# Kernel tuning notes

Hardware: AMD Instinct MI355X
Metric: run time of the kernel (lower is better)

## Reference

```python
import jax, jax.numpy as jnp
import numpy as np
import math

B, T, E = 1, 2048, 1024
H = 8                      # num_heads
D = E // H // 2            # head_dim = 64
LAMBDA_INIT = 0.8 - 0.6 * math.exp(-0.3 * 1)  # depth=1
SCALE_BASE = 512.0
THETA = 10000.0


def _rope_tables(T, d):
    # lucidrains rotary-embedding-torch, use_xpos=True, interleaved pairs
    inv_freq = 1.0 / (THETA ** (jnp.arange(0, d, 2, dtype=jnp.float32) / d))
    pos = jnp.arange(T, dtype=jnp.float32)
    freqs = pos[:, None] * inv_freq[None, :]            # (T, d/2)
    freqs = jnp.repeat(freqs, 2, axis=-1)               # (T, d) interleaved
    sv = (jnp.arange(0, d, 2, dtype=jnp.float32) + 0.4 * d) / (1.4 * d)
    power = (pos - T // 2) / SCALE_BASE
    scale = sv[None, :] ** power[:, None]               # (T, d/2)
    scale = jnp.concatenate([scale, scale], axis=-1)    # (T, d)
    return freqs, scale


def _rotate_half(x):
    # interleaved rotate: (..., d) pairs (x1, x2) -> (-x2, x1)
    x1 = x[..., 0::2]
    x2 = x[..., 1::2]
    return jnp.stack([-x2, x1], axis=-1).reshape(x.shape)


def _apply_rope(t, freqs, scale):
    # t: (B, T, h, d); freqs/scale: (T, d) broadcast over heads
    f = freqs[None, :, None, :]
    s = scale[None, :, None, :]
    return t * jnp.cos(f) * s + _rotate_half(t) * jnp.sin(f) * s


def setup_inputs() -> dict:
    key = jax.random.key(0)
    ks = jax.random.split(key, 9)
    w = 0.02
    return {
        "x": jax.random.normal(ks[0], (B, T, E), dtype=jnp.float32),
        "Wq": jax.random.normal(ks[1], (E, E), dtype=jnp.float32) * w,
        "Wk": jax.random.normal(ks[2], (E, E), dtype=jnp.float32) * w,
        "Wv": jax.random.normal(ks[3], (E, E), dtype=jnp.float32) * w,
        "Wo": jax.random.normal(ks[4], (E, E), dtype=jnp.float32) * w,
        "lambda_q1": jax.random.normal(ks[5], (D,), dtype=jnp.float32) * 0.1,
        "lambda_k1": jax.random.normal(ks[6], (D,), dtype=jnp.float32) * 0.1,
        "lambda_q2": jax.random.normal(ks[7], (D,), dtype=jnp.float32) * 0.1,
        "lambda_k2": jax.random.normal(ks[8], (D,), dtype=jnp.float32) * 0.1,
    }


def reference(x, Wq, Wk, Wv, Wo, lambda_q1, lambda_k1, lambda_q2, lambda_k2):
    b, t, e = x.shape
    scaling = D ** -0.5

    q = (x @ Wq.T).reshape(b, t, 2 * H, D)
    k = (x @ Wk.T).reshape(b, t, 2 * H, D)   # n_rep = 1
    v = (x @ Wv.T).reshape(b, t, H, 2 * D)

    freqs, scale = _rope_tables(t, D)
    q = _apply_rope(q, freqs, scale)
    k = _apply_rope(k, freqs, 1.0 / scale)   # xpos: keys use scale**-1

    q = jnp.transpose(q, (0, 2, 1, 3)) * scaling   # (B, 2H, T, D)
    k = jnp.transpose(k, (0, 2, 1, 3))             # (B, 2H, T, D)
    v = jnp.transpose(v, (0, 2, 1, 3))             # (B, H, T, 2D)

    scores = jnp.einsum('bhtd,bhsd->bhts', q, k)
    probs = jax.nn.softmax(scores.astype(jnp.float32), axis=-1).astype(scores.dtype)

    lam1 = jnp.exp(jnp.sum(lambda_q1 * lambda_k1))
    lam2 = jnp.exp(jnp.sum(lambda_q2 * lambda_k2))
    lam = lam1 - lam2 + LAMBDA_INIT

    probs = probs.reshape(b, H, 2, t, t)
    diff = probs[:, :, 0] - lam * probs[:, :, 1]   # (B, H, T, T)

    attn = jnp.einsum('bhts,bhsd->bhtd', diff, v)  # (B, H, T, 2D)
    # RMSNorm (no affine), eps=1e-5
    attn = attn * jax.lax.rsqrt(jnp.mean(attn * attn, axis=-1, keepdims=True) + 1e-5)
    attn = attn * (1.0 - LAMBDA_INIT)

    attn = jnp.transpose(attn, (0, 2, 1, 3)).reshape(b, t, e)
    return attn @ Wo.T
```

## Files before the change

kernel.cpp:

```cpp
#include <hip/hip_runtime.h>
#include <hip/hip_bf16.h>

typedef __hip_bfloat16 bf16;
typedef _Float16 f16;
typedef __attribute__((ext_vector_type(8))) __bf16 bf16x8;
typedef __attribute__((ext_vector_type(8))) _Float16 f16x8;
typedef __attribute__((ext_vector_type(4))) _Float16 f16x4;
typedef __attribute__((ext_vector_type(4))) float floatx4;
typedef __attribute__((ext_vector_type(16))) float floatx16;

#define T_SEQ 2048
#define EMB   1024
#define LAMBDA_INIT 0.35550906759096926f

__device__ __forceinline__ bf16 f2bf(float f) {
  unsigned u;
  __builtin_memcpy(&u, &f, 4);
  u += 0x7FFF + ((u >> 16) & 1);
  unsigned short h = (unsigned short)(u >> 16);
  bf16 r;
  __builtin_memcpy(&r, &h, 2);
  return r;
}

__device__ __forceinline__ int cvtpk_bf16(float lo, float hi) {
  int r;
  asm("v_cvt_pk_bf16_f32 %0, %1, %2" : "=v"(r) : "v"(lo), "v"(hi));
  return r;
}

__device__ __forceinline__ void permswap(int& a, int& b) {
  asm volatile("v_permlane32_swap_b32 %0, %1" : "+v"(a), "+v"(b));
}

__device__ __forceinline__ void gl_lds16(const void* g, void* l) {
  __builtin_amdgcn_global_load_lds((const __attribute__((address_space(1))) void*)g,
                                   (__attribute__((address_space(3))) void*)l, 16, 0, 0);
}

__device__ __forceinline__ floatx4 mfma_h(f16x8 a, f16x8 b, floatx4 c) {
  return __builtin_amdgcn_mfma_f32_16x16x32_f16(a, b, c, 0, 0, 0);
}
__device__ __forceinline__ floatx16 mfma32_h(f16x8 a, f16x8 b, floatx16 c) {
  return __builtin_amdgcn_mfma_f32_32x32x16_f16(a, b, c, 0, 0, 0);
}
__device__ __forceinline__ floatx16 mfma32_bf(bf16x8 a, bf16x8 b, floatx16 c) {
  return __builtin_amdgcn_mfma_f32_32x32x16_bf16(a, b, c, 0, 0, 0);
}

__global__ __launch_bounds__(256) void convert_kernel(
    const float* __restrict__ x,  const float* __restrict__ wq,
    const float* __restrict__ wk, const float* __restrict__ wv,
    const float* __restrict__ wo,
    f16* __restrict__ xf, f16* __restrict__ wqf, f16* __restrict__ wkf,
    f16* __restrict__ wvf, f16* __restrict__ wof)
{
  int b = blockIdx.x;
  const float* src; f16* dst; long off;
  if      (b < 2048) { src = x;  dst = xf;  off = (long)b * 1024; }
  else if (b < 3072) { src = wq; dst = wqf; off = (long)(b - 2048) * 1024; }
  else if (b < 4096) { src = wk; dst = wkf; off = (long)(b - 3072) * 1024; }
  else if (b < 5120) { src = wv; dst = wvf; off = (long)(b - 4096) * 1024; }
  else               { src = wo; dst = wof; off = (long)(b - 5120) * 1024; }
  long i = off + threadIdx.x * 4;
  float4 v = *(const float4*)(src + i);
  f16x4 o;
  o.x = (f16)v.x; o.y = (f16)v.y; o.z = (f16)v.z; o.w = (f16)v.w;
  *(f16x4*)(dst + i) = o;
}

template <int MODE>
__device__ __forceinline__ void gemm64x128_f16(
    const f16* __restrict__ A_, const f16* __restrict__ B_,
    void* C0v, int K, int ldc, int m0, int n0, char* smem)
{
  f16* As = (f16*)smem;
  f16* Bs = (f16*)(smem + 8192);
  const int tid  = threadIdx.x;
  const int wave = tid >> 6, lane = tid & 63, quad = lane >> 4, l16 = lane & 15;
  const int mo = (wave & 1) << 5;
  const int no = (wave >> 1) << 6;

  floatx4 acc[2][4];
  #pragma unroll
  for (int i = 0; i < 2; i++)
    #pragma unroll
    for (int j = 0; j < 4; j++) { acc[i][j][0]=0.f; acc[i][j][1]=0.f; acc[i][j][2]=0.f; acc[i][j][3]=0.f; }

  const int srow = tid >> 3;
  const int ch   = (tid & 7) ^ (srow & 7);
  const long aoff = (long)(m0 + srow) * K + ch * 8;
  const long boff = (long)(n0 + srow) * K + ch * 8;
  const int wb = wave << 10;

  for (int k0 = 0; k0 < K; k0 += 64) {
    #pragma unroll
    for (int rr = 0; rr < 2; rr++)
      gl_lds16(A_ + aoff + k0 + (long)rr * 32 * K, smem + wb + rr * 4096);
    #pragma unroll
    for (int rr = 0; rr < 4; rr++)
      gl_lds16(B_ + boff + k0 + (long)rr * 32 * K, smem + 8192 + wb + rr * 4096);
    __syncthreads();
    #pragma unroll
    for (int kt = 0; kt < 2; kt++) {
      f16x8 a[2], b[4];
      #pragma unroll
      for (int i = 0; i < 2; i++) {
        int m = mo + i * 16 + l16;
        a[i] = *(const f16x8*)(As + m * 64 + ((((kt << 2) | quad) ^ (m & 7)) << 3));
      }
      #pragma unroll
      for (int j = 0; j < 4; j++) {
        int n = no + j * 16 + l16;
        b[j] = *(const f16x8*)(Bs + n * 64 + ((((kt << 2) | quad) ^ (n & 7)) << 3));
      }
      #pragma unroll
      for (int i = 0; i < 2; i++)
        #pragma unroll
        for (int j = 0; j < 4; j++)
          acc[i][j] = mfma_h(a[i], b[j], acc[i][j]);
    }
    __syncthreads();
  }

  if (MODE == 1) {
    #pragma unroll
    for (int i = 0; i < 2; i++)
      #pragma unroll
      for (int j = 0; j < 4; j++)
        #pragma unroll
        for (int r = 0; r < 4; r++) {
          int row = m0 + mo + i * 16 + quad * 4 + r;
          int col = n0 + no + j * 16 + l16;
          ((float*)C0v)[(long)row * ldc + col] = acc[i][j][r];
        }
  } else {
    unsigned short* E = (unsigned short*)smem;
    #pragma unroll
    for (int i = 0; i < 2; i++)
      #pragma unroll
      for (int j = 0; j < 4; j++)
        #pragma unroll
        for (int r = 0; r < 4; r++) {
          int row = mo + i * 16 + quad * 4 + r;
          int col = no + j * 16 + l16;
          float v = acc[i][j][r];
          unsigned short bits;
          if (MODE == 0) {
            bf16 t = f2bf(v);
            __builtin_memcpy(&bits, &t, 2);
          } else {
            float p = __shfl_xor(v, 1, 64);
            int d = col & 63;
            float fr = (float)(m0 + row) * __expf((float)(d >> 1) * -0.28782313662425574f);
            float sn, cs;
            sincosf(fr, &sn, &cs);
            float rot = (col & 1) ? fmaf(v, cs, p * sn) : fmaf(v, cs, -p * sn);
            float power = (float)(m0 + row - 1024) * (1.0f / 512.0f);
            if (MODE == 3) power = -power;
            float sv = fmaf(2.0f, (float)(d & 31), 25.6f) * (1.0f / 89.6f);
            float s = __expf(power * __logf(sv));
            float ov = rot * s;
            if (MODE == 2) ov *= 0.125f;
            f16 t = (f16)ov;
            __builtin_memcpy(&bits, &t, 2);
          }
          E[row * 128 + col] = bits;
        }
    __syncthreads();
    const int rr0 = tid >> 4;
    const int c8  = (tid & 15) * 8;
    #pragma unroll
    for (int p2 = 0; p2 < 4; p2++) {
      int row = p2 * 16 + rr0;
      *(uint4*)((unsigned short*)C0v + (long)(m0 + row) * ldc + n0 + c8) =
          *(const uint4*)(E + row * 128 + c8);
    }
  }
}

__global__ __launch_bounds__(256) void qkv_gemm(
    const f16* __restrict__ xf,
    const f16* __restrict__ wqf, const f16* __restrict__ wkf,
    const f16* __restrict__ wvf,
    f16* __restrict__ qf, f16* __restrict__ kf, bf16* __restrict__ vt)
{
  __shared__ char smem[24576];
  int bid = blockIdx.x;
  if (bid < 256) {
    gemm64x128_f16<2>(xf, wqf, qf, 1024, 1024, (bid >> 3) * 64, (bid & 7) * 128, smem);
  } else if (bid < 512) {
    bid -= 256;
    gemm64x128_f16<3>(xf, wkf, kf, 1024, 1024, (bid >> 3) * 64, (bid & 7) * 128, smem);
  } else {
    bid -= 512;
    gemm64x128_f16<0>(wvf, xf, vt, 1024, 2048, (bid >> 4) * 64, (bid & 15) * 128, smem);
  }
}

__global__ __launch_bounds__(256) void out_gemm(const f16* __restrict__ attn,
                                                const f16* __restrict__ Wo,
                                                float* __restrict__ out)
{
  __shared__ char smem[24576];
  gemm64x128_f16<1>(attn, Wo, out, 1024, 1024,
                    (blockIdx.x >> 3) * 64, (blockIdx.x & 7) * 128, smem);
}

__global__ __launch_bounds__(256) void diff_attn(
    const f16* __restrict__ qf_, const f16* __restrict__ kf_,
    const bf16* __restrict__ vt,
    const float* __restrict__ lq1, const float* __restrict__ lk1,
    const float* __restrict__ lq2, const float* __restrict__ lk2,
    f16* __restrict__ attn)
{
  __shared__ char smem[65536];
  const int tid  = threadIdx.x;
  const int wave = tid >> 6, lane = tid & 63;
  const int l32 = lane & 31, lh = lane >> 5;
  const int h  = blockIdx.x & 7;
  const int qb = blockIdx.x >> 3;
  const int hl = wave >> 1;
  const int ws = wave & 1;
  const int hh = h * 2 + hl;
  const int t0 = qb * 32;

  float a1 = lq1[lane] * lk1[lane];
  float a2 = lq2[lane] * lk2[lane];
  #pragma unroll
  for (int off = 1; off < 64; off <<= 1) {
    a1 += __shfl_xor(a1, off, 64);
    a2 += __shfl_xor(a2, off, 64);
  }
  const float lam = __expf(a1) - __expf(a2) + LAMBDA_INIT;

  f16x8 qfr[4];
  {
    const f16* qrow = qf_ + (long)(t0 + l32) * EMB + hh * 64 + lh * 8;
    #pragma unroll
    for (int kt = 0; kt < 4; kt++) qfr[kt] = *(const f16x8*)(qrow + kt * 16);
  }

  floatx16 o[4];
  #pragma unroll
  for (int nt = 0; nt < 4; nt++)
    #pragma unroll
    for (int r = 0; r < 16; r++) o[nt][r] = 0.f;
  float lr = 0.f;

  const int srow = lane >> 3;
  const int ch   = (lane & 7) ^ srow;
  const f16*  kgp = kf_ + (long)(h * 2 + ws) * 64 + (long)srow * EMB + ch * 8;
  const bf16* vgp = vt + (long)(h * 128 + (wave - 2) * 64 + srow) * T_SEQ + ch * 8;
  const int kofs = wave * 8192;
  const int vofs = 16384 + (wave - 2) * 8192;

  if (wave < 2) {
    #pragma unroll
    for (int j = 0; j < 8; j++)
      gl_lds16(kgp + (long)j * 8 * EMB, smem + kofs + j * 1024);
  } else {
    #pragma unroll
    for (int j = 0; j < 8; j++)
      gl_lds16(vgp + (long)j * 8 * T_SEQ, smem + vofs + j * 1024);
  }

  for (int kb = 0; kb < T_SEQ; kb += 64) {
    const int cur = (kb >> 6) & 1;
    const char* sb = smem + cur * 32768;
    if (kb + 64 < T_SEQ) {
      char* nb = smem + (cur ^ 1) * 32768;
      if (wave < 2) {
        #pragma unroll
        for (int j = 0; j < 8; j++)
          gl_lds16(kgp + (long)(kb + 64) * EMB + (long)j * 8 * EMB,
                   nb + kofs + j * 1024);
      } else {
        #pragma unroll
        for (int j = 0; j < 8; j++)
          gl_lds16(vgp + (kb + 64) + (long)j * 8 * T_SEQ,
                   nb + vofs + j * 1024);
      }
      asm volatile("s_waitcnt vmcnt(8)" ::: "memory");
    } else {
      asm volatile("s_waitcnt vmcnt(0)" ::: "memory");
    }
    asm volatile("s_barrier" ::: "memory");

    const f16*  Ks  = (const f16*)(sb + hl * 8192);
    const bf16* Vsb = (const bf16*)(sb + 16384);

    floatx16 s;
    #pragma unroll
    for (int r = 0; r < 16; r++) s[r] = 0.f;
    #pragma unroll
    for (int kt = 0; kt < 4; kt++) {
      int krow = ws * 32 + l32;
      int c = kt * 2 + lh;
      f16x8 kfr = *(const f16x8*)(Ks + krow * 64 + ((c ^ (krow & 7)) << 3));
      s = mfma32_h(kfr, qfr[kt], s);
    }
    #pragma unroll
    for (int r = 0; r < 16; r++) {
      float pv = __builtin_amdgcn_exp2f(
          fmaf(s[r], 1.4426950408889634f, -17.312340490667562f));
      s[r] = pv;
      lr += pv;
    }
    bf16x8 pf[2];
    #pragma unroll
    for (int kt = 0; kt < 2; kt++) {
      const int b0 = kt * 8;
      int w0 = cvtpk_bf16(s[b0 + 0], s[b0 + 1]);
      int w1 = cvtpk_bf16(s[b0 + 2], s[b0 + 3]);
      int w2 = cvtpk_bf16(s[b0 + 4], s[b0 + 5]);
      int w3 = cvtpk_bf16(s[b0 + 6], s[b0 + 7]);
      permswap(w0, w2);
      permswap(w1, w3);
      union { int i[4]; bf16x8 v; } u;
      u.i[0] = w0; u.i[1] = w1; u.i[2] = w2; u.i[3] = w3;
      pf[kt] = u.v;
    }
    #pragma unroll
    for (int nt = 0; nt < 4; nt++) {
      #pragma unroll
      for (int kt = 0; kt < 2; kt++) {
        int vrow = nt * 32 + l32;
        int c = ws * 4 + kt * 2 + lh;
        bf16x8 vf = *(const bf16x8*)(Vsb + vrow * 64 + ((c ^ (vrow & 7)) << 3));
        o[nt] = mfma32_bf(pf[kt], vf, o[nt]);
      }
    }
    asm volatile("s_barrier" ::: "memory");
  }

  float lrw = lr + __shfl_xor(lr, 32, 64);

  float* Cb = (float*)smem;
  float* Lb = (float*)(smem + 32768);

  if (ws == 1) {
    #pragma unroll
    for (int r = 0; r < 16; r++) {
      int m = (r & 3) + 8 * (r >> 2) + 4 * lh;
      #pragma unroll
      for (int nt = 0; nt < 4; nt++)
        Cb[hl * 4096 + m * 128 + nt * 32 + l32] = o[nt][r];
    }
  }
  if (lh == 0) Lb[ws * 64 + hl * 32 + l32] = lrw;
  __syncthreads();
  if (ws == 0) {
    #pragma unroll
    for (int r = 0; r < 16; r++) {
      int m = (r & 3) + 8 * (r >> 2) + 4 * lh;
      float inv = 1.0f / (Lb[hl * 32 + m] + Lb[64 + hl * 32 + m]);
      #pragma unroll
      for (int nt = 0; nt < 4; nt++)
        o[nt][r] = (o[nt][r] + Cb[hl * 4096 + m * 128 + nt * 32 + l32]) * inv;
    }
  }
  __syncthreads();
  if (hl == 1 && ws == 0) {
    #pragma unroll
    for (int r = 0; r < 16; r++) {
      int m = (r & 3) + 8 * (r >> 2) + 4 * lh;
      #pragma unroll
      for (int nt = 0; nt < 4; nt++)
        Cb[4096 + m * 128 + nt * 32 + l32] = o[nt][r];
    }
  }
  __syncthreads();
  if (hl == 0 && ws == 0) {
    float ss[16];
    #pragma unroll
    for (int r = 0; r < 16; r++) {
      int m = (r & 3) + 8 * (r >> 2) + 4 * lh;
      ss[r] = 0.f;
      #pragma unroll
      for (int nt = 0; nt < 4; nt++) {
        float v = o[nt][r] - lam * Cb[4096 + m * 128 + nt * 32 + l32];
        o[nt][r] = v;
        ss[r] += v * v;
      }
    }
    #pragma unroll
    for (int r = 0; r < 16; r++) {
      ss[r] += __shfl_xor(ss[r], 1, 64);
      ss[r] += __shfl_xor(ss[r], 2, 64);
      ss[r] += __shfl_xor(ss[r], 4, 64);
      ss[r] += __shfl_xor(ss[r], 8, 64);
      ss[r] += __shfl_xor(ss[r], 16, 64);
      float rms = rsqrtf(ss[r] * (1.0f / 128.0f) + 1e-5f) * (1.0f - LAMBDA_INIT);
      int m = (r & 3) + 8 * (r >> 2) + 4 * lh;
      #pragma unroll
      for (int nt = 0; nt < 4; nt++)
        attn[(long)(t0 + m) * EMB + h * 128 + nt * 32 + l32] = (f16)(o[nt][r] * rms);
    }
  }
}

extern "C" void kernel_launch(void* const* d_in, const int* in_sizes, int n_in,
                              void* d_out, int out_size, void* d_ws, size_t ws_size,
                              hipStream_t stream)
{
  (void)in_sizes; (void)n_in; (void)out_size; (void)ws_size;
  const float* x   = (const float*)d_in[0];
  const float* Wq  = (const float*)d_in[1];
  const float* Wk  = (const float*)d_in[2];
  const float* Wv  = (const float*)d_in[3];
  const float* Wo  = (const float*)d_in[4];
  const float* lq1 = (const float*)d_in[5];
  const float* lk1 = (const float*)d_in[6];
  const float* lq2 = (const float*)d_in[7];
  const float* lk2 = (const float*)d_in[8];
  float* out = (float*)d_out;

  const size_t TM = (size_t)T_SEQ * EMB;
  const size_t WM = (size_t)EMB * EMB;
  bf16* vtws = (bf16*)d_ws;
  f16*  aws  = (f16*)(vtws + TM);
  f16*  xf   = aws  + TM;
  f16*  wqf  = xf   + TM;
  f16*  wkf  = wqf  + WM;
  f16*  wvf  = wkf  + WM;
  f16*  wof  = wvf  + WM;
  f16*  qf   = wof  + WM;
  f16*  kf   = qf   + TM;

  convert_kernel<<<6144, 256, 0, stream>>>(x, Wq, Wk, Wv, Wo,
                                           xf, wqf, wkf, wvf, wof);
  qkv_gemm<<<768, 256, 0, stream>>>(xf, wqf, wkf, wvf, qf, kf, vtws);
  diff_attn<<<512, 256, 0, stream>>>(qf, kf, vtws, lq1, lk1, lq2, lk2, aws);
  out_gemm<<<256, 256, 0, stream>>>(aws, wof, out);
}
```

Baseline: 173.5 us.

## Split diff-attention PV output columns across twice as many waves

The attention block grows from 4 to 8 waves. Each extra wave pair splits the 128-wide V output columns in half, so each wave holds two accumulator tiles instead of four. Loading of the K/V tiles is spread over all 8 waves, and the RMSNorm reduction now goes through shared memory. The aim is lower register pressure per wave and more waves to hide latency. The cost is that QK^T scores and the softmax exp are recomputed redundantly in both column halves, and there is an extra block sync.

```diff
diff --git a/kernel.cpp b/kernel.cpp
--- a/kernel.cpp
+++ b/kernel.cpp
@@ -207,7 +207,7 @@
                     (blockIdx.x >> 3) * 64, (blockIdx.x & 7) * 128, smem);
 }
 
-__global__ __launch_bounds__(256) void diff_attn(
+__global__ __launch_bounds__(512) void diff_attn(
     const f16* __restrict__ qf_, const f16* __restrict__ kf_,
     const bf16* __restrict__ vt,
     const float* __restrict__ lq1, const float* __restrict__ lk1,
@@ -220,8 +220,9 @@
   const int l32 = lane & 31, lh = lane >> 5;
   const int h  = blockIdx.x & 7;
   const int qb = blockIdx.x >> 3;
-  const int hl = wave >> 1;
-  const int ws = wave & 1;
+  const int hl = wave >> 2;
+  const int ws = (wave >> 1) & 1;
+  const int hf = wave & 1;
   const int hh = h * 2 + hl;
   const int t0 = qb * 32;
 
@@ -241,28 +242,28 @@
     for (int kt = 0; kt < 4; kt++) qfr[kt] = *(const f16x8*)(qrow + kt * 16);
   }
 
-  floatx16 o[4];
+  floatx16 o[2];
   #pragma unroll
-  for (int nt = 0; nt < 4; nt++)
-    #pragma unroll
-    for (int r = 0; r < 16; r++) o[nt][r] = 0.f;
+  for (int j2 = 0; j2 < 2; j2++)
+    #pragma unroll
+    for (int r = 0; r < 16; r++) o[j2][r] = 0.f;
   float lr = 0.f;
 
   const int srow = lane >> 3;
   const int ch   = (lane & 7) ^ srow;
-  const f16*  kgp = kf_ + (long)(h * 2 + ws) * 64 + (long)srow * EMB + ch * 8;
-  const bf16* vgp = vt + (long)(h * 128 + (wave - 2) * 64 + srow) * T_SEQ + ch * 8;
-  const int kofs = wave * 8192;
-  const int vofs = 16384 + (wave - 2) * 8192;
-
-  if (wave < 2) {
-    #pragma unroll
-    for (int j = 0; j < 8; j++)
-      gl_lds16(kgp + (long)j * 8 * EMB, smem + kofs + j * 1024);
+  const f16*  kgp = kf_ + (long)(h * 2 + (wave >> 1)) * 64 +
+                    (long)((wave & 1) * 32 + srow) * EMB + ch * 8;
+  const bf16* vgp = vt + (long)(h * 128 + (wave - 4) * 32 + srow) * T_SEQ + ch * 8;
+  const int sofs = (wave < 4) ? wave * 4096 : 16384 + (wave - 4) * 4096;
+
+  if (wave < 4) {
+    #pragma unroll
+    for (int j = 0; j < 4; j++)
+      gl_lds16(kgp + (long)j * 8 * EMB, smem + sofs + j * 1024);
   } else {
     #pragma unroll
-    for (int j = 0; j < 8; j++)
-      gl_lds16(vgp + (long)j * 8 * T_SEQ, smem + vofs + j * 1024);
+    for (int j = 0; j < 4; j++)
+      gl_lds16(vgp + (long)j * 8 * T_SEQ, smem + sofs + j * 1024);
   }
 
   for (int kb = 0; kb < T_SEQ; kb += 64) {
@@ -270,18 +271,18 @@
     const char* sb = smem + cur * 32768;
     if (kb + 64 < T_SEQ) {
       char* nb = smem + (cur ^ 1) * 32768;
-      if (wave < 2) {
-        #pragma unroll
-        for (int j = 0; j < 8; j++)
+      if (wave < 4) {
+        #pragma unroll
+        for (int j = 0; j < 4; j++)
           gl_lds16(kgp + (long)(kb + 64) * EMB + (long)j * 8 * EMB,
-                   nb + kofs + j * 1024);
+                   nb + sofs + j * 1024);
       } else {
         #pragma unroll
-        for (int j = 0; j < 8; j++)
+        for (int j = 0; j < 4; j++)
           gl_lds16(vgp + (kb + 64) + (long)j * 8 * T_SEQ,
-                   nb + vofs + j * 1024);
-      }
-      asm volatile("s_waitcnt vmcnt(8)" ::: "memory");
+                   nb + sofs + j * 1024);
+      }
+      asm volatile("s_waitcnt vmcnt(4)" ::: "memory");
     } else {
       asm volatile("s_waitcnt vmcnt(0)" ::: "memory");
     }
@@ -322,13 +323,13 @@
       pf[kt] = u.v;
     }
     #pragma unroll
-    for (int nt = 0; nt < 4; nt++) {
+    for (int j2 = 0; j2 < 2; j2++) {
       #pragma unroll
       for (int kt = 0; kt < 2; kt++) {
-        int vrow = nt * 32 + l32;
+        int vrow = (hf * 2 + j2) * 32 + l32;
         int c = ws * 4 + kt * 2 + lh;
         bf16x8 vf = *(const bf16x8*)(Vsb + vrow * 64 + ((c ^ (vrow & 7)) << 3));
-        o[nt] = mfma32_bf(pf[kt], vf, o[nt]);
+        o[j2] = mfma32_bf(pf[kt], vf, o[j2]);
       }
     }
     asm volatile("s_barrier" ::: "memory");
@@ -336,66 +337,77 @@
 
   float lrw = lr + __shfl_xor(lr, 32, 64);
 
-  float* Cb = (float*)smem;
-  float* Lb = (float*)(smem + 32768);
-
+  float* Cb  = (float*)smem;
+  float* O1  = (float*)(smem + 32768);
+  float* LbT = (float*)(smem + 49152);
+  float* SS  = (float*)(smem + 49664);
+
+  if (hf == 0 && lh == 0) LbT[(hl * 2 + ws) * 32 + l32] = lrw;
   if (ws == 1) {
     #pragma unroll
     for (int r = 0; r < 16; r++) {
       int m = (r & 3) + 8 * (r >> 2) + 4 * lh;
       #pragma unroll
-      for (int nt = 0; nt < 4; nt++)
-        Cb[hl * 4096 + m * 128 + nt * 32 + l32] = o[nt][r];
-    }
-  }
-  if (lh == 0) Lb[ws * 64 + hl * 32 + l32] = lrw;
+      for (int j2 = 0; j2 < 2; j2++)
+        Cb[(hl * 2 + hf) * 2048 + m * 64 + j2 * 32 + l32] = o[j2][r];
+    }
+  }
   __syncthreads();
   if (ws == 0) {
     #pragma unroll
     for (int r = 0; r < 16; r++) {
       int m = (r & 3) + 8 * (r >> 2) + 4 * lh;
-      float inv = 1.0f / (Lb[hl * 32 + m] + Lb[64 + hl * 32 + m]);
-      #pragma unroll
-      for (int nt = 0; nt < 4; nt++)
-        o[nt][r] = (o[nt][r] + Cb[hl * 4096 + m * 128 + nt * 32 + l32]) * inv;
-    }
-  }
-  __syncthreads();
-  if (hl == 1 && ws == 0) {
-    #pragma unroll
-    for (int r = 0; r < 16; r++) {
-      int m = (r & 3) + 8 * (r >> 2) + 4 * lh;
-      #pragma unroll
-      for (int nt = 0; nt < 4; nt++)
-        Cb[4096 + m * 128 + nt * 32 + l32] = o[nt][r];
+      float inv = 1.0f / (LbT[hl * 64 + m] + LbT[hl * 64 + 32 + m]);
+      #pragma unroll
+      for (int j2 = 0; j2 < 2; j2++)
+        o[j2][r] = (o[j2][r] + Cb[(hl * 2 + hf) * 2048 + m * 64 + j2 * 32 + l32]) * inv;
+    }
+    if (hl == 1) {
+      #pragma unroll
+      for (int r = 0; r < 16; r++) {
+        int m = (r & 3) + 8 * (r >> 2) + 4 * lh;
+        #pragma unroll
+        for (int j2 = 0; j2 < 2; j2++)
+          O1[hf * 2048 + m * 64 + j2 * 32 + l32] = o[j2][r];
+      }
     }
   }
   __syncthreads();
   if (hl == 0 && ws == 0) {
-    float ss[16];
+    float ssv[16];
     #pragma unroll
     for (int r = 0; r < 16; r++) {
       int m = (r & 3) + 8 * (r >> 2) + 4 * lh;
-      ss[r] = 0.f;
-      #pragma unroll
-      for (int nt = 0; nt < 4; nt++) {
-        float v = o[nt][r] - lam * Cb[4096 + m * 128 + nt * 32 + l32];
-        o[nt][r] = v;
-        ss[r] += v * v;
-      }
-    }
-    #pragma unroll
-    for (int r = 0; r < 16; r++) {
-      ss[r] += __shfl_xor(ss[r], 1, 64);
-      ss[r] += __shfl_xor(ss[r], 2, 64);
-      ss[r] += __shfl_xor(ss[r], 4, 64);
-      ss[r] += __shfl_xor(ss[r], 8, 64);
-      ss[r] += __shfl_xor(ss[r], 16, 64);
-      float rms = rsqrtf(ss[r] * (1.0f / 128.0f) + 1e-5f) * (1.0f - LAMBDA_INIT);
+      ssv[r] = 0.f;
+      #pragma unroll
+      for (int j2 = 0; j2 < 2; j2++) {
+        float v = o[j2][r] - lam * O1[hf * 2048 + m * 64 + j2 * 32 + l32];
+        o[j2][r] = v;
+        ssv[r] += v * v;
+      }
+    }
+    #pragma unroll
+    for (int r = 0; r < 16; r++) {
+      ssv[r] += __shfl_xor(ssv[r], 1, 64);
+      ssv[r] += __shfl_xor(ssv[r], 2, 64);
+      ssv[r] += __shfl_xor(ssv[r], 4, 64);
+      ssv[r] += __shfl_xor(ssv[r], 8, 64);
+      ssv[r] += __shfl_xor(ssv[r], 16, 64);
       int m = (r & 3) + 8 * (r >> 2) + 4 * lh;
-      #pragma unroll
-      for (int nt = 0; nt < 4; nt++)
-        attn[(long)(t0 + m) * EMB + h * 128 + nt * 32 + l32] = (f16)(o[nt][r] * rms);
+      if (l32 == 0) SS[hf * 32 + m] = ssv[r];
+    }
+  }
+  __syncthreads();
+  if (hl == 0 && ws == 0) {
+    #pragma unroll
+    for (int r = 0; r < 16; r++) {
+      int m = (r & 3) + 8 * (r >> 2) + 4 * lh;
+      float sstot = SS[m] + SS[32 + m];
+      float rms = rsqrtf(sstot * (1.0f / 128.0f) + 1e-5f) * (1.0f - LAMBDA_INIT);
+      #pragma unroll
+      for (int j2 = 0; j2 < 2; j2++)
+        attn[(long)(t0 + m) * EMB + h * 128 + (hf * 2 + j2) * 32 + l32] =
+            (f16)(o[j2][r] * rms);
     }
   }
 }
@@ -431,6 +443,6 @@
   convert_kernel<<<6144, 256, 0, stream>>>(x, Wq, Wk, Wv, Wo,
                                            xf, wqf, wkf, wvf, wof);
   qkv_gemm<<<768, 256, 0, stream>>>(xf, wqf, wkf, wvf, qf, kf, vtws);
-  diff_attn<<<512, 256, 0, stream>>>(qf, kf, vtws, lq1, lk1, lq2, lk2, aws);
+  diff_attn<<<512, 512, 0, stream>>>(qf, kf, vtws, lq1, lk1, lq2, lk2, aws);
   out_gemm<<<256, 256, 0, stream>>>(aws, wof, out);
 }
```

Result: slower. 180.0 us (+3.8%).
